# Performance work log

Measured on AMD Instinct MI355X. Metric: run time of the kernel, lower is better.

The kernel has to match this reference:

```python
import math
import jax, jax.numpy as jnp
import numpy as np

B, S, OBS, ACT, D, H, F, L = 4, 512, 64, 16, 1024, 16, 4096, 4
T = 2 * S - 1  # 1023


def setup_inputs() -> dict:
    key = jax.random.key(0)
    ks = iter(jax.random.split(key, 48))
    def nrm(shape, scale=0.02):
        return (jax.random.normal(next(ks), shape, dtype=jnp.float32) * scale)
    z = lambda *s: jnp.zeros(s, jnp.float32)
    o = lambda *s: jnp.ones(s, jnp.float32)
    inp = {
        'observations': jax.random.normal(next(ks), (B, S, OBS), jnp.float32),
        'actions': jax.random.normal(next(ks), (B, S - 1, ACT), jnp.float32),
        # input_fc: obs_size -> D -> D -> D
        'in_w1': nrm((OBS, D)), 'in_b1': z(D), 'in_w2': nrm((D, D)), 'in_b2': z(D), 'in_w3': nrm((D, D)), 'in_b3': z(D),
        # action_fc: action_size -> D -> D -> D
        'act_w1': nrm((ACT, D)), 'act_b1': z(D), 'act_w2': nrm((D, D)), 'act_b2': z(D), 'act_w3': nrm((D, D)), 'act_b3': z(D),
        # output_fc: D -> D -> D -> action_size
        'out_w1': nrm((D, D)), 'out_b1': z(D), 'out_w2': nrm((D, D)), 'out_b2': z(D), 'out_w3': nrm((D, ACT)), 'out_b3': z(ACT),
        # decoder self-attn (stacked over L layers)
        'sa_w_in': nrm((L, D, 3 * D)), 'sa_b_in': z(L, 3 * D), 'sa_w_out': nrm((L, D, D)), 'sa_b_out': z(L, D),
        # decoder cross-attn
        'ca_w_in': nrm((L, D, 3 * D)), 'ca_b_in': z(L, 3 * D), 'ca_w_out': nrm((L, D, D)), 'ca_b_out': z(L, D),
        # decoder FFN
        'ff_w1': nrm((L, D, F)), 'ff_b1': z(L, F), 'ff_w2': nrm((L, F, D)), 'ff_b2': z(L, D),
        # layer norms
        'ln1_g': o(L, D), 'ln1_b': z(L, D), 'ln2_g': o(L, D), 'ln2_b': z(L, D), 'ln3_g': o(L, D), 'ln3_b': z(L, D),
        'lnf_g': o(D), 'lnf_b': z(D),
    }
    return inp


def _mlp(x, w1, b1, w2, b2, w3, b3):
    x = jax.nn.relu(x @ w1 + b1)
    x = jax.nn.relu(x @ w2 + b2)
    return x @ w3 + b3


def _ln(x, g, b, eps=1e-5):
    mu = x.mean(-1, keepdims=True)
    var = ((x - mu) ** 2).mean(-1, keepdims=True)
    return (x - mu) * jax.lax.rsqrt(var + eps) * g + b


def _mha(q_in, kv_in, w_in, b_in, w_out, b_out, mask):
    Bq, Tq, Dm = q_in.shape
    Tk = kv_in.shape[1]
    dh = Dm // H
    q = q_in @ w_in[:, :Dm] + b_in[:Dm]
    k = kv_in @ w_in[:, Dm:2 * Dm] + b_in[Dm:2 * Dm]
    v = kv_in @ w_in[:, 2 * Dm:] + b_in[2 * Dm:]
    q = q.reshape(Bq, Tq, H, dh).transpose(0, 2, 1, 3)
    k = k.reshape(Bq, Tk, H, dh).transpose(0, 2, 1, 3)
    v = v.reshape(Bq, Tk, H, dh).transpose(0, 2, 1, 3)
    s = jnp.einsum('bhqd,bhkd->bhqk', q, k) / math.sqrt(dh)
    if mask is not None:
        s = s + mask
    a = jax.nn.softmax(s, axis=-1)
    out = jnp.einsum('bhqk,bhkd->bhqd', a, v).transpose(0, 2, 1, 3).reshape(Bq, Tq, Dm)
    return out @ w_out + b_out


def reference(observations, actions,
              in_w1, in_b1, in_w2, in_b2, in_w3, in_b3,
              act_w1, act_b1, act_w2, act_b2, act_w3, act_b3,
              out_w1, out_b1, out_w2, out_b2, out_w3, out_b3,
              sa_w_in, sa_b_in, sa_w_out, sa_b_out,
              ca_w_in, ca_b_in, ca_w_out, ca_b_out,
              ff_w1, ff_b1, ff_w2, ff_b2,
              ln1_g, ln1_b, ln2_g, ln2_b, ln3_g, ln3_b, lnf_g, lnf_b):
    obs_tok = _mlp(observations, in_w1, in_b1, in_w2, in_b2, in_w3, in_b3)   # [B,S,D]
    act_tok = _mlp(actions, act_w1, act_b1, act_w2, act_b2, act_w3, act_b3)  # [B,S-1,D]
    # fused interleave [obs1, act1, obs2, ..., obsS] (replaces the python loops)
    tgt = jnp.zeros((B, T, D), obs_tok.dtype).at[:, 0::2].set(obs_tok).at[:, 1::2].set(act_tok)
    # PositionalEncoding is applied on a batch-first tensor in the original code,
    # so pe[:x.size(0)] indexes by BATCH and broadcasts over the sequence dim (bug-faithful).
    pos = jnp.arange(B, dtype=jnp.float32)[:, None]
    div = jnp.exp(jnp.arange(0, D, 2, dtype=jnp.float32) * (-math.log(10000.0) / D))
    pe = jnp.stack([jnp.sin(pos * div), jnp.cos(pos * div)], axis=-1).reshape(B, D)
    x = tgt + pe[:, None, :]
    mask = jnp.triu(jnp.full((T, T), -jnp.inf, dtype=jnp.float32), k=1)
    mem = jnp.zeros((B, 1, D), x.dtype)  # inp_tok (zero memory token)
    for l in range(L):  # post-norm nn.TransformerDecoderLayer, dropout=0
        x = _ln(x + _mha(x, x, sa_w_in[l], sa_b_in[l], sa_w_out[l], sa_b_out[l], mask), ln1_g[l], ln1_b[l])
        x = _ln(x + _mha(x, mem, ca_w_in[l], ca_b_in[l], ca_w_out[l], ca_b_out[l], None), ln2_g[l], ln2_b[l])
        ff = jax.nn.relu(x @ ff_w1[l] + ff_b1[l]) @ ff_w2[l] + ff_b2[l]
        x = _ln(x + ff, ln3_g[l], ln3_b[l])
    x = _ln(x, lnf_g, lnf_b)  # nn.Transformer final decoder norm
    return _mlp(x, out_w1, out_b1, out_w2, out_b2, out_w3, out_b3)  # [B,T,action_size]
```

## Files before the change

kernel.cpp:

```cpp
#include <hip/hip_runtime.h>
#include <hip/hip_bf16.h>
#include <cstdint>
#include <cstddef>

#define B_  4
#define S_  512
#define T_  1023
#define D_  1024
#define H_  16
#define DH_ 64
#define F_  4096
#define L_  4

typedef float f32x4 __attribute__((ext_vector_type(4)));
typedef __bf16 bf16x8 __attribute__((ext_vector_type(8)));

__device__ inline unsigned pack_bf2(float a, float b) {
    union { __hip_bfloat16 h; unsigned short u; } ua, ub;
    ua.h = __float2bfloat16(a); ub.h = __float2bfloat16(b);
    return (unsigned)ua.u | ((unsigned)ub.u << 16);
}

__global__ __launch_bounds__(256) void gemm_bf16(
    const __hip_bfloat16* __restrict__ A, const __hip_bfloat16* __restrict__ Wt,
    const float* __restrict__ bias,
    float* __restrict__ Cf, __hip_bfloat16* __restrict__ Cb,
    int M, int K, int N, int relu, int ksplit)
{
    __shared__ __align__(16) __hip_bfloat16 Asm0[128 * 32];
    __shared__ __align__(16) __hip_bfloat16 Bsm0[128 * 32];
    __shared__ __align__(16) __hip_bfloat16 Asm1[128 * 32];
    __shared__ __align__(16) __hip_bfloat16 Bsm1[128 * 32];
    const int tid  = threadIdx.x;
    const int lane = tid & 63;
    const int w    = tid >> 6;
    const int wr   = w >> 1, wc = w & 1;
    const int l15  = lane & 15, l4 = lane >> 4;

    const int gx = gridDim.x;
    int bid = blockIdx.y * gx + blockIdx.x;
    {
        const int nwg = gx * gridDim.y;
        const int q = nwg >> 3, r = nwg & 7;
        const int xcd = bid & 7, idx = bid >> 3;
        bid = (xcd < r ? xcd * (q + 1) : r * (q + 1) + (xcd - r) * q) + idx;
    }
    const int row0 = (bid / gx) * 128;
    const int col0 = (bid % gx) * 128;
    const int z = blockIdx.z;
    const int kslice = K / ksplit;
    const int kbase = z * kslice;

    f32x4 acc[4][4] = {};

    auto stage = [&](__hip_bfloat16* As, __hip_bfloat16* Bs, int kt) {
        auto* ldsA = (__attribute__((address_space(3))) char*)As;
        auto* ldsB = (__attribute__((address_space(3))) char*)Bs;
        #pragma unroll
        for (int half = 0; half < 2; ++half) {
            const int ch = half * 256 + tid;
            const int r  = ch >> 2;
            const int c  = (ch & 3) * 8;
            int gr = row0 + r; gr = (gr < M) ? gr : (M - 1);
            const __hip_bfloat16* srcA = A + (size_t)gr * K + kt + c;
            __builtin_amdgcn_global_load_lds(
                (const __attribute__((address_space(1))) unsigned*)srcA,
                (__attribute__((address_space(3))) unsigned*)(ldsA + (size_t)ch * 16),
                16, 0, 0);
            int gc = col0 + r; gc = (gc < N) ? gc : (N - 1);
            const __hip_bfloat16* srcB = Wt + (size_t)gc * K + kt + c;
            __builtin_amdgcn_global_load_lds(
                (const __attribute__((address_space(1))) unsigned*)srcB,
                (__attribute__((address_space(3))) unsigned*)(ldsB + (size_t)ch * 16),
                16, 0, 0);
        }
    };
    auto compute = [&](const __hip_bfloat16* As, const __hip_bfloat16* Bs) {
        const __hip_bfloat16* ab = As + (size_t)(wr * 64 + l15) * 32 + l4 * 8;
        const __hip_bfloat16* bb = Bs + (size_t)(wc * 64 + l15) * 32 + l4 * 8;
        bf16x8 af[4], bf[4];
        #pragma unroll
        for (int mi = 0; mi < 4; ++mi) af[mi] = *(const bf16x8*)(ab + mi * 16 * 32);
        #pragma unroll
        for (int nj = 0; nj < 4; ++nj) bf[nj] = *(const bf16x8*)(bb + nj * 16 * 32);
        #pragma unroll
        for (int mi = 0; mi < 4; ++mi)
            #pragma unroll
            for (int nj = 0; nj < 4; ++nj)
                acc[mi][nj] = __builtin_amdgcn_mfma_f32_16x16x32_bf16(
                    af[mi], bf[nj], acc[mi][nj], 0, 0, 0);
    };

    const int nk = kslice >> 5;
    stage(Asm0, Bsm0, kbase);
    __syncthreads();
    for (int t = 0; t < nk; t += 2) {
        if (t + 1 < nk) stage(Asm1, Bsm1, kbase + (t + 1) * 32);
        compute(Asm0, Bsm0);
        __syncthreads();
        if (t + 1 < nk) {
            if (t + 2 < nk) stage(Asm0, Bsm0, kbase + (t + 2) * 32);
            compute(Asm1, Bsm1);
            __syncthreads();
        }
    }

    if (ksplit > 1) {
        float* dst = Cf + (size_t)z * M * N;
        #pragma unroll
        for (int nj = 0; nj < 4; ++nj) {
            const int c = col0 + wc * 64 + nj * 16 + l15;
            if (c >= N) continue;
            #pragma unroll
            for (int mi = 0; mi < 4; ++mi)
                #pragma unroll
                for (int i = 0; i < 4; ++i) {
                    const int r = row0 + wr * 64 + mi * 16 + l4 * 4 + i;
                    if (r < M) dst[(size_t)r * N + c] = acc[mi][nj][i];
                }
        }
    } else {
        #pragma unroll
        for (int nj = 0; nj < 4; ++nj) {
            const int c = col0 + wc * 64 + nj * 16 + l15;
            if (c >= N) continue;
            const float bv = bias[c];
            #pragma unroll
            for (int mi = 0; mi < 4; ++mi)
                #pragma unroll
                for (int i = 0; i < 4; ++i) {
                    const int r = row0 + wr * 64 + mi * 16 + l4 * 4 + i;
                    if (r >= M) continue;
                    float v = acc[mi][nj][i] + bv;
                    if (relu) v = fmaxf(v, 0.f);
                    if (Cf) Cf[(size_t)r * N + c] = v;
                    if (Cb) Cb[(size_t)r * N + c] = __float2bfloat16(v);
                }
        }
    }
}

__global__ __launch_bounds__(256) void reduce_split(
    const float* __restrict__ part, int SK, size_t pstride,
    const float* __restrict__ bias, int N, int total4, int relu,
    float* __restrict__ outf, __hip_bfloat16* __restrict__ outb)
{
    const int idx4 = blockIdx.x * 256 + threadIdx.x;
    if (idx4 >= total4) return;
    const size_t base = (size_t)idx4 * 4;
    const int c = (int)(base & (size_t)(N - 1));
    float4 v = *(const float4*)(part + base);
    for (int s = 1; s < SK; ++s) {
        const float4 p = *(const float4*)(part + (size_t)s * pstride + base);
        v.x += p.x; v.y += p.y; v.z += p.z; v.w += p.w;
    }
    const float4 bv = *(const float4*)(bias + c);
    v.x += bv.x; v.y += bv.y; v.z += bv.z; v.w += bv.w;
    if (relu) {
        v.x = fmaxf(v.x, 0.f); v.y = fmaxf(v.y, 0.f);
        v.z = fmaxf(v.z, 0.f); v.w = fmaxf(v.w, 0.f);
    }
    if (outf) *(float4*)(outf + base) = v;
    if (outb) {
        __hip_bfloat16* o = outb + base;
        o[0] = __float2bfloat16(v.x); o[1] = __float2bfloat16(v.y);
        o[2] = __float2bfloat16(v.z); o[3] = __float2bfloat16(v.w);
    }
}

__global__ __launch_bounds__(256) void transpose_w(
    const float* __restrict__ W, __hip_bfloat16* __restrict__ Wt,
    int K, int N, int Kpad)
{
    __shared__ float t[32][33];
    W  += (size_t)blockIdx.z * K * N;
    Wt += (size_t)blockIdx.z * N * Kpad;
    const int n0 = blockIdx.x * 32, k0 = blockIdx.y * 32;
    const int tx = threadIdx.x & 31, ty = threadIdx.x >> 5;
    #pragma unroll
    for (int i = 0; i < 4; ++i) {
        int r = ty + i * 8;
        int k = k0 + r, n = n0 + tx;
        t[r][tx] = (k < K && n < N) ? W[(size_t)k * N + n] : 0.f;
    }
    __syncthreads();
    #pragma unroll
    for (int i = 0; i < 4; ++i) {
        int r = ty + i * 8;
        int n = n0 + r, k = k0 + tx;
        if (n < N && k < Kpad) Wt[(size_t)n * Kpad + k] = __float2bfloat16(t[tx][r]);
    }
}

__global__ __launch_bounds__(256) void convert_pad(
    const float* __restrict__ in, __hip_bfloat16* __restrict__ out,
    int M, int Kin, int Kout)
{
    int idx = blockIdx.x * 256 + threadIdx.x;
    if (idx >= M * Kout) return;
    int r = idx / Kout, c = idx - r * Kout;
    out[idx] = __float2bfloat16(c < Kin ? in[(size_t)r * Kin + c] : 0.f);
}

__global__ __launch_bounds__(256) void v_transpose(
    const __hip_bfloat16* __restrict__ qkvb, __hip_bfloat16* __restrict__ vt)
{
    __shared__ __hip_bfloat16 tile[32][33];
    const int b  = blockIdx.z;
    const int c0 = blockIdx.x * 32;
    const int t0 = blockIdx.y * 32;
    const int tx = threadIdx.x & 31, ty = threadIdx.x >> 5;
    const __hip_bfloat16 z = __float2bfloat16(0.f);
    #pragma unroll
    for (int i = 0; i < 4; ++i) {
        const int tl = ty + i * 8;
        const int t = t0 + tl;
        tile[tl][tx] = (t < T_) ? qkvb[(size_t)(b * T_ + t) * 3072 + 2048 + c0 + tx] : z;
    }
    __syncthreads();
    #pragma unroll
    for (int i = 0; i < 4; ++i) {
        const int cl = ty + i * 8;
        const int t = t0 + tx;
        vt[((size_t)(b * 1024 + c0 + cl)) * 1024 + t] = (t < T_) ? tile[tx][cl] : z;
    }
}

__global__ __launch_bounds__(256) void attn_mfma(
    const __hip_bfloat16* __restrict__ qkvb,
    const __hip_bfloat16* __restrict__ vt,
    __hip_bfloat16* __restrict__ out)
{
    __shared__ __align__(16) __hip_bfloat16 Qs[2][128][32];
    __shared__ __align__(16) __hip_bfloat16 Ks[2][64][32];
    __shared__ __align__(16) __hip_bfloat16 Vs[2][64][32];
    __shared__ __align__(16) __hip_bfloat16 Ps[4][2][32][32];
    __shared__ float Lw[4][2][16];

    const int bh = blockIdx.x;
    const int b = bh >> 4, h = bh & 15;
    const int q0 = blockIdx.y * 128;
    const int tid = threadIdx.x;
    const int w = tid >> 6, lane = tid & 63;
    const int l15 = lane & 15, l4 = lane >> 4;
    const size_t ldq = 3 * D_;

    {
        #pragma unroll
        for (int c = 0; c < 2; ++c)
            #pragma unroll
            for (int it = 0; it < 2; ++it) {
                const int ch = it * 256 + tid;
                const int r = ch >> 2, cp = ch & 3;
                int qr = q0 + r; qr = (qr < T_) ? qr : (T_ - 1);
                const __hip_bfloat16* src = qkvb + (size_t)(b * T_ + qr) * ldq + h * 64 + c * 32 + cp * 8;
                __builtin_amdgcn_global_load_lds(
                    (const __attribute__((address_space(1))) unsigned*)src,
                    (__attribute__((address_space(3))) unsigned*)((__attribute__((address_space(3))) char*)&Qs[c][0][0] + ch * 16),
                    16, 0, 0);
            }
    }
    __syncthreads();
    bf16x8 qreg[2][2];
    #pragma unroll
    for (int qf = 0; qf < 2; ++qf)
        #pragma unroll
        for (int c = 0; c < 2; ++c)
            qreg[qf][c] = *(const bf16x8*)&Qs[c][w * 32 + qf * 16 + l15][l4 * 8];

    f32x4 of[2][4] = {};
    float lp[2] = {0.f, 0.f};
    const int qmaxw = q0 + w * 32 + 31;
    const int kend = (q0 + 128 < T_) ? (q0 + 128) : T_;

    for (int k0 = 0; k0 < kend; k0 += 64) {
        __syncthreads();
        {
            const int r = tid >> 2, cp = tid & 3;
            #pragma unroll
            for (int c = 0; c < 2; ++c) {
                int kr = k0 + r; kr = (kr < T_) ? kr : (T_ - 1);
                const __hip_bfloat16* srcK = qkvb + (size_t)(b * T_ + kr) * ldq + D_ + h * 64 + c * 32 + cp * 8;
                __builtin_amdgcn_global_load_lds(
                    (const __attribute__((address_space(1))) unsigned*)srcK,
                    (__attribute__((address_space(3))) unsigned*)((__attribute__((address_space(3))) char*)&Ks[c][0][0] + tid * 16),
                    16, 0, 0);
                const __hip_bfloat16* srcV = vt + ((size_t)(b * 1024 + h * 64 + r)) * 1024 + k0 + c * 32 + cp * 8;
                __builtin_amdgcn_global_load_lds(
                    (const __attribute__((address_space(1))) unsigned*)srcV,
                    (__attribute__((address_space(3))) unsigned*)((__attribute__((address_space(3))) char*)&Vs[c][0][0] + tid * 16),
                    16, 0, 0);
            }
        }
        __syncthreads();

        if (k0 <= qmaxw) {
            f32x4 sf[4][2] = {};
            #pragma unroll
            for (int c = 0; c < 2; ++c) {
                bf16x8 kf[4];
                #pragma unroll
                for (int kfr = 0; kfr < 4; ++kfr)
                    kf[kfr] = *(const bf16x8*)&Ks[c][kfr * 16 + l15][l4 * 8];
                #pragma unroll
                for (int kfr = 0; kfr < 4; ++kfr)
                    #pragma unroll
                    for (int qf = 0; qf < 2; ++qf)
                        sf[kfr][qf] = __builtin_amdgcn_mfma_f32_16x16x32_bf16(
                            kf[kfr], qreg[qf][c], sf[kfr][qf], 0, 0, 0);
            }
            const bool needmask = (k0 + 63) > (q0 + w * 32);
            #pragma unroll
            for (int kfr = 0; kfr < 4; ++kfr) {
                #pragma unroll
                for (int qf = 0; qf < 2; ++qf) {
                    const int qg = q0 + w * 32 + qf * 16 + l15;
                    float p[4];
                    #pragma unroll
                    for (int i = 0; i < 4; ++i) {
                        const int kg = k0 + kfr * 16 + l4 * 4 + i;
                        float pv = __expf(sf[kfr][qf][i] * 0.125f);
                        if (needmask && kg > qg) pv = 0.f;
                        p[i] = pv;
                        lp[qf] += pv;
                    }
                    unsigned* dst = (unsigned*)&Ps[w][kfr >> 1][qf * 16 + l15][(kfr & 1) * 16 + l4 * 4];
                    dst[0] = pack_bf2(p[0], p[1]);
                    dst[1] = pack_bf2(p[2], p[3]);
                }
            }
            #pragma unroll
            for (int kc = 0; kc < 2; ++kc) {
                bf16x8 pa[2], vb[4];
                #pragma unroll
                for (int qf = 0; qf < 2; ++qf)
                    pa[qf] = *(const bf16x8*)&Ps[w][kc][qf * 16 + l15][l4 * 8];
                #pragma unroll
                for (int df = 0; df < 4; ++df)
                    vb[df] = *(const bf16x8*)&Vs[kc][df * 16 + l15][l4 * 8];
                #pragma unroll
                for (int qf = 0; qf < 2; ++qf)
                    #pragma unroll
                    for (int df = 0; df < 4; ++df)
                        of[qf][df] = __builtin_amdgcn_mfma_f32_16x16x32_bf16(
                            pa[qf], vb[df], of[qf][df], 0, 0, 0);
            }
        }
    }

    #pragma unroll
    for (int qf = 0; qf < 2; ++qf) {
        float v = lp[qf];
        v += __shfl_xor(v, 16);
        v += __shfl_xor(v, 32);
        if (l4 == 0) Lw[w][qf][l15] = v;
    }
    __syncthreads();
    #pragma unroll
    for (int qf = 0; qf < 2; ++qf) {
        float inv[4];
        #pragma unroll
        for (int i = 0; i < 4; ++i) inv[i] = 1.f / Lw[w][qf][l4 * 4 + i];
        #pragma unroll
        for (int df = 0; df < 4; ++df) {
            #pragma unroll
            for (int i = 0; i < 4; ++i) {
                const int qg = q0 + w * 32 + qf * 16 + l4 * 4 + i;
                if (qg < T_)
                    out[(size_t)(b * T_ + qg) * D_ + h * 64 + df * 16 + l15] =
                        __float2bfloat16(of[qf][df][i] * inv[i]);
            }
        }
    }
}

__device__ inline void block_ln_stats(float4 v, float& mu, float& inv,
                                      float* ws, float* ws2, float* mu_s, float* inv_s)
{
    const int tid = threadIdx.x;
    float s  = v.x + v.y + v.z + v.w;
    float s2 = v.x * v.x + v.y * v.y + v.z * v.z + v.w * v.w;
    #pragma unroll
    for (int off = 32; off; off >>= 1) {
        s  += __shfl_down(s, off);
        s2 += __shfl_down(s2, off);
    }
    const int wid = tid >> 6;
    if ((tid & 63) == 0) { ws[wid] = s; ws2[wid] = s2; }
    __syncthreads();
    if (tid == 0) {
        float S  = ws[0] + ws[1] + ws[2] + ws[3];
        float S2 = ws2[0] + ws2[1] + ws2[2] + ws2[3];
        float m = S * (1.f / (float)D_);
        float var = S2 * (1.f / (float)D_) - m * m;
        *mu_s = m;
        *inv_s = rsqrtf(var + 1e-5f);
    }
    __syncthreads();
    mu = *mu_s; inv = *inv_s;
}

__global__ __launch_bounds__(256) void add_ln_kernel(
    float* __restrict__ x, const float* __restrict__ p, int SK, size_t pstride,
    const float* __restrict__ pbias,
    const float* __restrict__ g, const float* __restrict__ beta,
    __hip_bfloat16* __restrict__ xb)
{
    const int row = blockIdx.x;
    const int tid = threadIdx.x;
    __shared__ float ws[4], ws2[4], mu_s, inv_s;
    float4* xr = reinterpret_cast<float4*>(x + (size_t)row * D_);
    float4 v = xr[tid];
    if (p) {
        for (int s = 0; s < SK; ++s) {
            const float4 wv = reinterpret_cast<const float4*>(
                p + (size_t)s * pstride + (size_t)row * D_)[tid];
            v.x += wv.x; v.y += wv.y; v.z += wv.z; v.w += wv.w;
        }
        if (pbias) {
            const float4 bv = reinterpret_cast<const float4*>(pbias)[tid];
            v.x += bv.x; v.y += bv.y; v.z += bv.z; v.w += bv.w;
        }
    }
    float mu, inv;
    block_ln_stats(v, mu, inv, ws, ws2, &mu_s, &inv_s);
    const float4 gg = reinterpret_cast<const float4*>(g)[tid];
    const float4 bb = reinterpret_cast<const float4*>(beta)[tid];
    float4 o;
    o.x = (v.x - mu) * inv * gg.x + bb.x;
    o.y = (v.y - mu) * inv * gg.y + bb.y;
    o.z = (v.z - mu) * inv * gg.z + bb.z;
    o.w = (v.w - mu) * inv * gg.w + bb.w;
    xr[tid] = o;
    if (xb) {
        __hip_bfloat16* xo = xb + (size_t)row * D_ + tid * 4;
        xo[0] = __float2bfloat16(o.x);
        xo[1] = __float2bfloat16(o.y);
        xo[2] = __float2bfloat16(o.z);
        xo[3] = __float2bfloat16(o.w);
    }
}

__global__ __launch_bounds__(256) void add_ln2_kernel(
    float* __restrict__ x, const float* __restrict__ p, int SK, size_t pstride,
    const float* __restrict__ pbias, const float* __restrict__ cav,
    const float* __restrict__ g1, const float* __restrict__ b1,
    const float* __restrict__ g2, const float* __restrict__ b2,
    __hip_bfloat16* __restrict__ xb)
{
    const int row = blockIdx.x;
    const int tid = threadIdx.x;
    __shared__ float ws[4], ws2[4], mu_s, inv_s;
    float4* xr = reinterpret_cast<float4*>(x + (size_t)row * D_);
    float4 v = xr[tid];
    for (int s = 0; s < SK; ++s) {
        const float4 wv = reinterpret_cast<const float4*>(
            p + (size_t)s * pstride + (size_t)row * D_)[tid];
        v.x += wv.x; v.y += wv.y; v.z += wv.z; v.w += wv.w;
    }
    if (pbias) {
        const float4 bv = reinterpret_cast<const float4*>(pbias)[tid];
        v.x += bv.x; v.y += bv.y; v.z += bv.z; v.w += bv.w;
    }
    float mu, inv;
    block_ln_stats(v, mu, inv, ws, ws2, &mu_s, &inv_s);
    const float4 g1v = reinterpret_cast<const float4*>(g1)[tid];
    const float4 b1v = reinterpret_cast<const float4*>(b1)[tid];
    const float4 cv  = reinterpret_cast<const float4*>(cav)[tid];
    float4 u;
    u.x = (v.x - mu) * inv * g1v.x + b1v.x + cv.x;
    u.y = (v.y - mu) * inv * g1v.y + b1v.y + cv.y;
    u.z = (v.z - mu) * inv * g1v.z + b1v.z + cv.z;
    u.w = (v.w - mu) * inv * g1v.w + b1v.w + cv.w;
    __syncthreads();
    float mu2, inv2;
    block_ln_stats(u, mu2, inv2, ws, ws2, &mu_s, &inv_s);
    const float4 g2v = reinterpret_cast<const float4*>(g2)[tid];
    const float4 b2v = reinterpret_cast<const float4*>(b2)[tid];
    float4 o;
    o.x = (u.x - mu2) * inv2 * g2v.x + b2v.x;
    o.y = (u.y - mu2) * inv2 * g2v.y + b2v.y;
    o.z = (u.z - mu2) * inv2 * g2v.z + b2v.z;
    o.w = (u.w - mu2) * inv2 * g2v.w + b2v.w;
    xr[tid] = o;
    __hip_bfloat16* xo = xb + (size_t)row * D_ + tid * 4;
    xo[0] = __float2bfloat16(o.x);
    xo[1] = __float2bfloat16(o.y);
    xo[2] = __float2bfloat16(o.z);
    xo[3] = __float2bfloat16(o.w);
}

__global__ __launch_bounds__(256) void interleave_pe_kernel(
    const float* __restrict__ obs_tok, const float* __restrict__ act_tok,
    float* __restrict__ x, __hip_bfloat16* __restrict__ xb)
{
    const int row = blockIdx.x;
    const int b = row / T_;
    const int t = row - b * T_;
    const float* src = (t & 1)
        ? (act_tok + (size_t)(b * (S_ - 1) + (t >> 1)) * D_)
        : (obs_tok + (size_t)(b * S_ + (t >> 1)) * D_);
    float* xr = x + (size_t)row * D_;
    __hip_bfloat16* xo = xb + (size_t)row * D_;
    #pragma unroll
    for (int k = 0; k < 4; ++k) {
        int d = threadIdx.x + k * 256;
        float ang = (float)b * expf(-(float)(d & ~1) * (9.210340371976184f / 1024.0f));
        float pe = (d & 1) ? cosf(ang) : sinf(ang);
        float v = src[d] + pe;
        xr[d] = v;
        xo[d] = __float2bfloat16(v);
    }
}

__global__ __launch_bounds__(256) void ca_part_kernel(
    const float* __restrict__ ca_b_in, const float* __restrict__ ca_w_out,
    float* __restrict__ part)
{
    const int idx = blockIdx.x * 256 + threadIdx.x;
    const int ks = blockIdx.y;
    const int l = idx >> 10, d = idx & 1023;
    const float* bv = ca_b_in + (size_t)l * 3 * D_ + 2 * D_ + ks * 64;
    const float* wp = ca_w_out + (size_t)l * D_ * D_ + (size_t)(ks * 64) * D_ + d;
    float s = 0.f;
    #pragma unroll 8
    for (int k = 0; k < 64; ++k) s = fmaf(bv[k], wp[(size_t)k * D_], s);
    part[(size_t)ks * (L_ * D_) + idx] = s;
}

__global__ __launch_bounds__(256) void ca_reduce_kernel(
    const float* __restrict__ part, const float* __restrict__ ca_b_out,
    float* __restrict__ out)
{
    const int idx = blockIdx.x * 256 + threadIdx.x;
    float s = ca_b_out[idx];
    #pragma unroll
    for (int ks = 0; ks < 16; ++ks) s += part[(size_t)ks * (L_ * D_) + idx];
    out[idx] = s;
}

extern "C" void kernel_launch(void* const* d_in, const int* in_sizes, int n_in,
                              void* d_out, int out_size, void* d_ws, size_t ws_size,
                              hipStream_t stream)
{
    const float* obs     = (const float*)d_in[0];
    const float* act     = (const float*)d_in[1];
    const float* in_w1   = (const float*)d_in[2];
    const float* in_b1   = (const float*)d_in[3];
    const float* in_w2   = (const float*)d_in[4];
    const float* in_b2   = (const float*)d_in[5];
    const float* in_w3   = (const float*)d_in[6];
    const float* in_b3   = (const float*)d_in[7];
    const float* act_w1  = (const float*)d_in[8];
    const float* act_b1  = (const float*)d_in[9];
    const float* act_w2  = (const float*)d_in[10];
    const float* act_b2  = (const float*)d_in[11];
    const float* act_w3  = (const float*)d_in[12];
    const float* act_b3  = (const float*)d_in[13];
    const float* out_w1  = (const float*)d_in[14];
    const float* out_b1  = (const float*)d_in[15];
    const float* out_w2  = (const float*)d_in[16];
    const float* out_b2  = (const float*)d_in[17];
    const float* out_w3  = (const float*)d_in[18];
    const float* out_b3  = (const float*)d_in[19];
    const float* sa_w_in = (const float*)d_in[20];
    const float* sa_b_in = (const float*)d_in[21];
    const float* sa_w_out= (const float*)d_in[22];
    const float* sa_b_out= (const float*)d_in[23];
    const float* ca_b_in = (const float*)d_in[25];
    const float* ca_w_out= (const float*)d_in[26];
    const float* ca_b_out= (const float*)d_in[27];
    const float* ff_w1   = (const float*)d_in[28];
    const float* ff_b1   = (const float*)d_in[29];
    const float* ff_w2   = (const float*)d_in[30];
    const float* ff_b2   = (const float*)d_in[31];
    const float* ln1_g   = (const float*)d_in[32];
    const float* ln1_b   = (const float*)d_in[33];
    const float* ln2_g   = (const float*)d_in[34];
    const float* ln2_b   = (const float*)d_in[35];
    const float* ln3_g   = (const float*)d_in[36];
    const float* ln3_b   = (const float*)d_in[37];
    const float* lnf_g   = (const float*)d_in[38];
    const float* lnf_b   = (const float*)d_in[39];

    const int MT = B_ * T_;
    const int Mo = B_ * S_;
    const int Ma = B_ * (S_ - 1);

    char* base = (char*)d_ws;
    size_t used = 0;
    auto alloc = [&](size_t bytes) -> char* {
        char* r = base + used;
        used += (bytes + 255) & ~(size_t)255;
        return r;
    };
    typedef __hip_bfloat16 bf;
    bf* wi1  = (bf*)alloc((size_t)1024 * 64 * 2);
    bf* wi2  = (bf*)alloc((size_t)1024 * 1024 * 2);
    bf* wi3  = (bf*)alloc((size_t)1024 * 1024 * 2);
    bf* wa1  = (bf*)alloc((size_t)1024 * 32 * 2);
    bf* wa2  = (bf*)alloc((size_t)1024 * 1024 * 2);
    bf* wa3  = (bf*)alloc((size_t)1024 * 1024 * 2);
    bf* wo1  = (bf*)alloc((size_t)1024 * 1024 * 2);
    bf* wo2  = (bf*)alloc((size_t)1024 * 1024 * 2);
    bf* wo3  = (bf*)alloc((size_t)16 * 1024 * 2);
    bf* wsin = (bf*)alloc((size_t)L_ * 3072 * 1024 * 2);
    bf* wsout= (bf*)alloc((size_t)L_ * 1024 * 1024 * 2);
    bf* wf1  = (bf*)alloc((size_t)L_ * 4096 * 1024 * 2);
    bf* wf2  = (bf*)alloc((size_t)L_ * 1024 * 4096 * 2);
    bf* obs_bf = (bf*)alloc((size_t)Mo * 64 * 2);
    bf* act_bf = (bf*)alloc((size_t)Ma * 32 * 2);
    bf* x_bf   = (bf*)alloc((size_t)MT * D_ * 2);
    bf* attnb  = (bf*)alloc((size_t)MT * D_ * 2);
    bf* h1b    = (bf*)alloc((size_t)MT * D_ * 2);
    bf* h2b    = (bf*)alloc((size_t)MT * D_ * 2);
    char* shared_rg = alloc((size_t)MT * F_ * 2);
    bf* qkvb = (bf*)shared_rg;
    bf* ffh  = (bf*)shared_rg;
    bf* vt   = (bf*)alloc((size_t)B_ * 1024 * 1024 * 2);
    float* x       = (float*)alloc((size_t)MT * D_ * 4);
    float* y       = (float*)alloc((size_t)MT * D_ * 4);
    float* obs_tok = (float*)alloc((size_t)Mo * D_ * 4);
    float* act_tok = (float*)alloc((size_t)Ma * D_ * 4);
    float* ca      = (float*)alloc((size_t)L_ * D_ * 4);
    float* ca_part = (float*)alloc((size_t)16 * L_ * D_ * 4);
    if (used > ws_size) return;
    float* part_loop = y;
    float* part_pre  = (float*)shared_rg;
    float* part_post = (float*)shared_rg;

    auto tw = [&](const float* W, bf* Wt, int K, int N, int Kpad, int batch) {
        dim3 g((N + 31) / 32, (Kpad + 31) / 32, batch);
        transpose_w<<<g, 256, 0, stream>>>(W, Wt, K, N, Kpad);
    };
    auto gemm = [&](const bf* A, const bf* Wt, const float* bias,
                    float* Cf, bf* Cb, int M, int K, int N, int relu, int sk) {
        dim3 g((N + 127) / 128, (M + 127) / 128, sk);
        gemm_bf16<<<g, 256, 0, stream>>>(A, Wt, bias, Cf, Cb, M, K, N, relu, sk);
    };
    auto gemm_red = [&](const bf* A, const bf* Wt, const float* bias,
                        float* Cf, bf* Cb, int M, int K, int N, int relu, int sk,
                        float* part) {
        if (sk <= 1) { gemm(A, Wt, bias, Cf, Cb, M, K, N, relu, 1); return; }
        gemm(A, Wt, nullptr, part, nullptr, M, K, N, 0, sk);
        const size_t MN = (size_t)M * N;
        const int total4 = (int)(MN / 4);
        reduce_split<<<(total4 + 255) / 256, 256, 0, stream>>>(
            part, sk, MN, bias, N, total4, relu, Cf, Cb);
    };

    tw(in_w1,  wi1, 64,   1024, 64,   1);
    tw(in_w2,  wi2, 1024, 1024, 1024, 1);
    tw(in_w3,  wi3, 1024, 1024, 1024, 1);
    tw(act_w1, wa1, 16,   1024, 32,   1);
    tw(act_w2, wa2, 1024, 1024, 1024, 1);
    tw(act_w3, wa3, 1024, 1024, 1024, 1);
    tw(out_w1, wo1, 1024, 1024, 1024, 1);
    tw(out_w2, wo2, 1024, 1024, 1024, 1);
    tw(out_w3, wo3, 1024, 16,   1024, 1);
    tw(sa_w_in,  wsin,  1024, 3072, 1024, L_);
    tw(sa_w_out, wsout, 1024, 1024, 1024, L_);
    tw(ff_w1,    wf1,   1024, 4096, 1024, L_);
    tw(ff_w2,    wf2,   4096, 1024, 4096, L_);

    convert_pad<<<(Mo * 64 + 255) / 256, 256, 0, stream>>>(obs, obs_bf, Mo, 64, 64);
    convert_pad<<<(Ma * 32 + 255) / 256, 256, 0, stream>>>(act, act_bf, Ma, 16, 32);
    ca_part_kernel<<<dim3((L_ * D_) / 256, 16), 256, 0, stream>>>(ca_b_in, ca_w_out, ca_part);
    ca_reduce_kernel<<<(L_ * D_) / 256, 256, 0, stream>>>(ca_part, ca_b_out, ca);

    gemm(obs_bf, wi1, in_b1, nullptr, h1b, Mo, 64, D_, 1, 1);
    gemm_red(h1b, wi2, in_b2, nullptr, h2b, Mo, D_, D_, 1, 4, part_pre);
    gemm_red(h2b, wi3, in_b3, obs_tok, nullptr, Mo, D_, D_, 0, 4, part_pre);
    gemm(act_bf, wa1, act_b1, nullptr, h1b, Ma, 32, D_, 1, 1);
    gemm_red(h1b, wa2, act_b2, nullptr, h2b, Ma, D_, D_, 1, 4, part_pre);
    gemm_red(h2b, wa3, act_b3, act_tok, nullptr, Ma, D_, D_, 0, 4, part_pre);

    interleave_pe_kernel<<<MT, 256, 0, stream>>>(obs_tok, act_tok, x, x_bf);

    for (int l = 0; l < L_; ++l) {
        gemm(x_bf, wsin + (size_t)l * 3072 * 1024, sa_b_in + (size_t)l * 3 * D_,
             nullptr, qkvb, MT, D_, 3 * D_, 0, 1);
        v_transpose<<<dim3(32, 32, B_), 256, 0, stream>>>(qkvb, vt);
        attn_mfma<<<dim3(B_ * H_, 8), 256, 0, stream>>>(qkvb, vt, attnb);
        gemm(attnb, wsout + (size_t)l * 1024 * 1024, nullptr,
             part_loop, nullptr, MT, D_, D_, 0, 2);
        add_ln2_kernel<<<MT, 256, 0, stream>>>(x, part_loop, 2, (size_t)MT * D_,
             sa_b_out + (size_t)l * D_, ca + (size_t)l * D_,
             ln1_g + (size_t)l * D_, ln1_b + (size_t)l * D_,
             ln2_g + (size_t)l * D_, ln2_b + (size_t)l * D_, x_bf);
        gemm(x_bf, wf1 + (size_t)l * 4096 * 1024, ff_b1 + (size_t)l * F_,
             nullptr, ffh, MT, D_, F_, 1, 1);
        gemm(ffh, wf2 + (size_t)l * 1024 * 4096, nullptr,
             part_loop, nullptr, MT, F_, D_, 0, 2);
        add_ln_kernel<<<MT, 256, 0, stream>>>(x, part_loop, 2, (size_t)MT * D_,
             ff_b2 + (size_t)l * D_,
             ln3_g + (size_t)l * D_, ln3_b + (size_t)l * D_, x_bf);
    }

    add_ln_kernel<<<MT, 256, 0, stream>>>(x, nullptr, 0, 0, nullptr, lnf_g, lnf_b, x_bf);
    gemm_red(x_bf, wo1, out_b1, nullptr, h1b, MT, D_, D_, 1, 2, part_post);
    gemm_red(h1b,  wo2, out_b2, nullptr, h2b, MT, D_, D_, 1, 2, part_post);
    gemm_red(h2b,  wo3, out_b3, (float*)d_out, nullptr, MT, D_, 16, 0, 8, part_post);
}
```

Before: 1.478 ms.

## Triple-buffer GEMM LDS pipeline and split FFN down-projection four ways

The GEMM main loop moves from a double-buffered LDS scheme with two full __syncthreads per pair of k-steps to a three-stage ring. It uses explicit vmcnt waits and a single s_barrier per step, so global loads for step t+2 overlap compute on step t. Separately, when workspace allows, the FFN second GEMM uses split-K of 4 instead of 2, writing the extra partials to a new buffer that add_ln sums. The goal is to hide load latency and raise occupancy for the long-K GEMM, at the cost of more LDS per block, extra partial-sum traffic, and reliance on hand-tuned waitcnt values matching the stage's load count.

Measured after the change: 1.486 ms. No clear change (+0.5%).

```diff
diff --git a/kernel.cpp b/kernel.cpp
--- a/kernel.cpp
+++ b/kernel.cpp
@@ -24,13 +24,12 @@
 __global__ __launch_bounds__(256) void gemm_bf16(
     const __hip_bfloat16* __restrict__ A, const __hip_bfloat16* __restrict__ Wt,
     const float* __restrict__ bias,
-    float* __restrict__ Cf, __hip_bfloat16* __restrict__ Cb,
+    float* __restrict__ Cf, float* __restrict__ Cf2,
+    __hip_bfloat16* __restrict__ Cb,
     int M, int K, int N, int relu, int ksplit)
 {
-    __shared__ __align__(16) __hip_bfloat16 Asm0[128 * 32];
-    __shared__ __align__(16) __hip_bfloat16 Bsm0[128 * 32];
-    __shared__ __align__(16) __hip_bfloat16 Asm1[128 * 32];
-    __shared__ __align__(16) __hip_bfloat16 Bsm1[128 * 32];
+    __shared__ __align__(16) __hip_bfloat16 AsmB[3][128 * 32];
+    __shared__ __align__(16) __hip_bfloat16 BsmB[3][128 * 32];
     const int tid  = threadIdx.x;
     const int lane = tid & 63;
     const int w    = tid >> 6;
@@ -92,21 +91,26 @@
     };
 
     const int nk = kslice >> 5;
-    stage(Asm0, Bsm0, kbase);
-    __syncthreads();
-    for (int t = 0; t < nk; t += 2) {
-        if (t + 1 < nk) stage(Asm1, Bsm1, kbase + (t + 1) * 32);
-        compute(Asm0, Bsm0);
-        __syncthreads();
+    __hip_bfloat16 *A0 = AsmB[0], *A1 = AsmB[1], *A2 = AsmB[2];
+    __hip_bfloat16 *B0 = BsmB[0], *B1 = BsmB[1], *B2 = BsmB[2];
+    stage(A0, B0, kbase);
+    if (nk > 1) stage(A1, B1, kbase + 32);
+    for (int t = 0; t < nk; ++t) {
         if (t + 1 < nk) {
-            if (t + 2 < nk) stage(Asm0, Bsm0, kbase + (t + 2) * 32);
-            compute(Asm1, Bsm1);
-            __syncthreads();
-        }
+            asm volatile("s_waitcnt vmcnt(4)" ::: "memory");
+        } else {
+            asm volatile("s_waitcnt vmcnt(0)" ::: "memory");
+        }
+        __builtin_amdgcn_s_barrier();
+        if (t + 2 < nk) stage(A2, B2, kbase + (t + 2) * 32);
+        compute(A0, B0);
+        __hip_bfloat16* ta = A0; A0 = A1; A1 = A2; A2 = ta;
+        __hip_bfloat16* tb = B0; B0 = B1; B1 = B2; B2 = tb;
     }
 
     if (ksplit > 1) {
-        float* dst = Cf + (size_t)z * M * N;
+        const size_t MN = (size_t)M * N;
+        float* dst = (z < 2) ? (Cf + (size_t)z * MN) : (Cf2 + (size_t)(z - 2) * MN);
         #pragma unroll
         for (int nj = 0; nj < 4; ++nj) {
             const int c = col0 + wc * 64 + nj * 16 + l15;
@@ -141,7 +145,8 @@
 }
 
 __global__ __launch_bounds__(256) void reduce_split(
-    const float* __restrict__ part, int SK, size_t pstride,
+    const float* __restrict__ part, const float* __restrict__ part2,
+    int SK, size_t pstride,
     const float* __restrict__ bias, int N, int total4, int relu,
     float* __restrict__ outf, __hip_bfloat16* __restrict__ outb)
 {
@@ -151,7 +156,9 @@
     const int c = (int)(base & (size_t)(N - 1));
     float4 v = *(const float4*)(part + base);
     for (int s = 1; s < SK; ++s) {
-        const float4 p = *(const float4*)(part + (size_t)s * pstride + base);
+        const float* src = (s < 2) ? (part + (size_t)s * pstride)
+                                   : (part2 + (size_t)(s - 2) * pstride);
+        const float4 p = *(const float4*)(src + base);
         v.x += p.x; v.y += p.y; v.z += p.z; v.w += p.w;
     }
     const float4 bv = *(const float4*)(bias + c);
@@ -401,8 +408,8 @@
 }
 
 __global__ __launch_bounds__(256) void add_ln_kernel(
-    float* __restrict__ x, const float* __restrict__ p, int SK, size_t pstride,
-    const float* __restrict__ pbias,
+    float* __restrict__ x, const float* __restrict__ p, const float* __restrict__ p2,
+    int SK, size_t pstride, const float* __restrict__ pbias,
     const float* __restrict__ g, const float* __restrict__ beta,
     __hip_bfloat16* __restrict__ xb)
 {
@@ -413,8 +420,9 @@
     float4 v = xr[tid];
     if (p) {
         for (int s = 0; s < SK; ++s) {
-            const float4 wv = reinterpret_cast<const float4*>(
-                p + (size_t)s * pstride + (size_t)row * D_)[tid];
+            const float* src = (s < 2) ? (p + (size_t)s * pstride)
+                                       : (p2 + (size_t)(s - 2) * pstride);
+            const float4 wv = reinterpret_cast<const float4*>(src + (size_t)row * D_)[tid];
             v.x += wv.x; v.y += wv.y; v.z += wv.z; v.w += wv.w;
         }
         if (pbias) {
@@ -628,25 +636,29 @@
     float* part_loop = y;
     float* part_pre  = (float*)shared_rg;
     float* part_post = (float*)shared_rg;
+    float* part_extra = (float*)(base + used);
+    const size_t extra_bytes = (size_t)2 * MT * D_ * 4;
+    const int ES4 = (used + extra_bytes <= ws_size) ? 1 : 0;
 
     auto tw = [&](const float* W, bf* Wt, int K, int N, int Kpad, int batch) {
         dim3 g((N + 31) / 32, (Kpad + 31) / 32, batch);
         transpose_w<<<g, 256, 0, stream>>>(W, Wt, K, N, Kpad);
     };
     auto gemm = [&](const bf* A, const bf* Wt, const float* bias,
-                    float* Cf, bf* Cb, int M, int K, int N, int relu, int sk) {
+                    float* Cf, float* Cf2, bf* Cb,
+                    int M, int K, int N, int relu, int sk) {
         dim3 g((N + 127) / 128, (M + 127) / 128, sk);
-        gemm_bf16<<<g, 256, 0, stream>>>(A, Wt, bias, Cf, Cb, M, K, N, relu, sk);
+        gemm_bf16<<<g, 256, 0, stream>>>(A, Wt, bias, Cf, Cf2, Cb, M, K, N, relu, sk);
     };
     auto gemm_red = [&](const bf* A, const bf* Wt, const float* bias,
                         float* Cf, bf* Cb, int M, int K, int N, int relu, int sk,
                         float* part) {
-        if (sk <= 1) { gemm(A, Wt, bias, Cf, Cb, M, K, N, relu, 1); return; }
-        gemm(A, Wt, nullptr, part, nullptr, M, K, N, 0, sk);
+        if (sk <= 1) { gemm(A, Wt, bias, Cf, nullptr, Cb, M, K, N, relu, 1); return; }
         const size_t MN = (size_t)M * N;
+        gemm(A, Wt, nullptr, part, part + 2 * MN, nullptr, M, K, N, 0, sk);
         const int total4 = (int)(MN / 4);
         reduce_split<<<(total4 + 255) / 256, 256, 0, stream>>>(
-            part, sk, MN, bias, N, total4, relu, Cf, Cb);
+            part, part + 2 * MN, sk, MN, bias, N, total4, relu, Cf, Cb);
     };
 
     tw(in_w1,  wi1, 64,   1024, 64,   1);
@@ -668,10 +680,10 @@
     ca_part_kernel<<<dim3((L_ * D_) / 256, 16), 256, 0, stream>>>(ca_b_in, ca_w_out, ca_part);
     ca_reduce_kernel<<<(L_ * D_) / 256, 256, 0, stream>>>(ca_part, ca_b_out, ca);
 
-    gemm(obs_bf, wi1, in_b1, nullptr, h1b, Mo, 64, D_, 1, 1);
+    gemm(obs_bf, wi1, in_b1, nullptr, nullptr, h1b, Mo, 64, D_, 1, 1);
     gemm_red(h1b, wi2, in_b2, nullptr, h2b, Mo, D_, D_, 1, 4, part_pre);
     gemm_red(h2b, wi3, in_b3, obs_tok, nullptr, Mo, D_, D_, 0, 4, part_pre);
-    gemm(act_bf, wa1, act_b1, nullptr, h1b, Ma, 32, D_, 1, 1);
+    gemm(act_bf, wa1, act_b1, nullptr, nullptr, h1b, Ma, 32, D_, 1, 1);
     gemm_red(h1b, wa2, act_b2, nullptr, h2b, Ma, D_, D_, 1, 4, part_pre);
     gemm_red(h2b, wa3, act_b3, act_tok, nullptr, Ma, D_, D_, 0, 4, part_pre);
 
@@ -679,25 +691,34 @@
 
     for (int l = 0; l < L_; ++l) {
         gemm(x_bf, wsin + (size_t)l * 3072 * 1024, sa_b_in + (size_t)l * 3 * D_,
-             nullptr, qkvb, MT, D_, 3 * D_, 0, 1);
+             nullptr, nullptr, qkvb, MT, D_, 3 * D_, 0, 1);
         v_transpose<<<dim3(32, 32, B_), 256, 0, stream>>>(qkvb, vt);
         attn_mfma<<<dim3(B_ * H_, 8), 256, 0, stream>>>(qkvb, vt, attnb);
         gemm(attnb, wsout + (size_t)l * 1024 * 1024, nullptr,
-             part_loop, nullptr, MT, D_, D_, 0, 2);
+             part_loop, nullptr, nullptr, MT, D_, D_, 0, 2);
         add_ln2_kernel<<<MT, 256, 0, stream>>>(x, part_loop, 2, (size_t)MT * D_,
              sa_b_out + (size_t)l * D_, ca + (size_t)l * D_,
              ln1_g + (size_t)l * D_, ln1_b + (size_t)l * D_,
              ln2_g + (size_t)l * D_, ln2_b + (size_t)l * D_, x_bf);
         gemm(x_bf, wf1 + (size_t)l * 4096 * 1024, ff_b1 + (size_t)l * F_,
-             nullptr, ffh, MT, D_, F_, 1, 1);
-        gemm(ffh, wf2 + (size_t)l * 1024 * 4096, nullptr,
-             part_loop, nullptr, MT, F_, D_, 0, 2);
-        add_ln_kernel<<<MT, 256, 0, stream>>>(x, part_loop, 2, (size_t)MT * D_,
-             ff_b2 + (size_t)l * D_,
-             ln3_g + (size_t)l * D_, ln3_b + (size_t)l * D_, x_bf);
-    }
-
-    add_ln_kernel<<<MT, 256, 0, stream>>>(x, nullptr, 0, 0, nullptr, lnf_g, lnf_b, x_bf);
+             nullptr, nullptr, ffh, MT, D_, F_, 1, 1);
+        if (ES4) {
+            gemm(ffh, wf2 + (size_t)l * 1024 * 4096, nullptr,
+                 part_loop, part_extra, nullptr, MT, F_, D_, 0, 4);
+            add_ln_kernel<<<MT, 256, 0, stream>>>(x, part_loop, part_extra, 4,
+                 (size_t)MT * D_, ff_b2 + (size_t)l * D_,
+                 ln3_g + (size_t)l * D_, ln3_b + (size_t)l * D_, x_bf);
+        } else {
+            gemm(ffh, wf2 + (size_t)l * 1024 * 4096, nullptr,
+                 part_loop, nullptr, nullptr, MT, F_, D_, 0, 2);
+            add_ln_kernel<<<MT, 256, 0, stream>>>(x, part_loop, part_loop, 2,
+                 (size_t)MT * D_, ff_b2 + (size_t)l * D_,
+                 ln3_g + (size_t)l * D_, ln3_b + (size_t)l * D_, x_bf);
+        }
+    }
+
+    add_ln_kernel<<<MT, 256, 0, stream>>>(x, nullptr, nullptr, 0, 0, nullptr,
+                                          lnf_g, lnf_b, x_bf);
     gemm_red(x_bf, wo1, out_b1, nullptr, h1b, MT, D_, D_, 1, 2, part_post);
     gemm_red(h1b,  wo2, out_b2, nullptr, h2b, MT, D_, D_, 1, 2, part_post);
     gemm_red(h2b,  wo3, out_b3, (float*)d_out, nullptr, MT, D_, 16, 0, 8, part_post);
```
